# Kernel tuning notes

Hardware: AMD Instinct MI355X
Metric: run time of the kernel (lower is better)

The kernel has to match this reference:

```python
import jax, jax.numpy as jnp
import numpy as np
from jax import lax

N = 100000
G = 256          # voxel grid extent per axis
MULT = 8
C_HID = 32 * MULT  # 256
K3 = 27


def setup_inputs() -> dict:
    key = jax.random.key(0)
    k_feat, k1, k2, k3, k4 = jax.random.split(key, 5)
    # unique voxel coordinates in a G^3 grid (sparse tensors have no duplicate coords)
    rng = np.random.default_rng(0)
    lin = rng.choice(G * G * G, size=N, replace=False)
    coords = np.stack([lin // (G * G), (lin // G) % G, lin % G], axis=1).astype(np.int32)
    feats = jax.random.normal(k_feat, (N, 2), dtype=jnp.float32)
    def w(k, cin, cout):
        return jax.random.normal(k, (K3, cin, cout), dtype=jnp.float32) / np.sqrt(K3 * cin)
    return {
        "coords": jnp.asarray(coords),
        "feats": feats,
        "W1": w(k1, 2, C_HID),
        "W2": w(k2, C_HID, C_HID),
        "W3": w(k3, C_HID, C_HID),
        "W4": w(k4, C_HID, 2),
    }


def _neighbor_map(coords):
    """Kernel map for a 3x3x3 stride-1 sparse conv: for each of 27 offsets and each
    point i, the index j of the point at coords[i]+offset (and a validity mask).
    Built once and shared by all four layers (stride=1 preserves coordinates)."""
    S = G + 2  # pad linearization base so offsets in {-1,0,1} never wrap
    c = coords.astype(jnp.int32) + 1
    keys = (c[:, 0] * S + c[:, 1]) * S + c[:, 2]            # [N]
    order = jnp.argsort(keys)
    skeys = keys[order]
    offs = jnp.array([[dx, dy, dz] for dx in (-1, 0, 1)
                      for dy in (-1, 0, 1) for dz in (-1, 0, 1)], dtype=jnp.int32)  # [27,3]
    nc = c[None, :, :] + offs[:, None, :]                    # [27,N,3]
    qk = (nc[..., 0] * S + nc[..., 1]) * S + nc[..., 2]      # [27,N]
    pos = jnp.clip(jnp.searchsorted(skeys, qk), 0, N - 1)
    valid = skeys[pos] == qk                                 # [27,N]
    idx = order[pos]                                         # [27,N]
    return idx, valid


def _sparse_conv(feats, W, idx, valid):
    """gather -> GEMM -> accumulate, scanned over the 27 kernel offsets."""
    out0 = jnp.zeros((feats.shape[0], W.shape[-1]), feats.dtype)
    def step(acc, kv):
        i, v, w = kv
        g = jnp.where(v[:, None], feats[i], 0.0)   # [N,Cin] gathered neighbor feats
        return acc + g @ w, None
    out, _ = lax.scan(step, out0, (idx, valid, W))
    return out


def reference(coords, feats, W1, W2, W3, W4):
    idx, valid = _neighbor_map(coords)
    x = _sparse_conv(feats, W1, idx, valid)
    x = _sparse_conv(x, W2, idx, valid)
    x = _sparse_conv(x, W3, idx, valid)
    x = _sparse_conv(x, W4, idx, valid)
    return x
```

## Files before the change

### kernel.cpp

```cpp
#include <hip/hip_runtime.h>

#define HASH_BITS 19
#define HASH_SIZE (1u << HASH_BITS)
#define HASH_MASK (HASH_SIZE - 1)
#define EMPTY64 0xFFFFFFFFFFFFFFFFull
#define CH 256
#define PCH 32
#define NREP 8
#define NSEG (27 * NREP)
#define SEGCAP 4096
#define BM_WORDS 536704

typedef __attribute__((ext_vector_type(8))) short short8;
typedef __attribute__((ext_vector_type(4))) float floatx4;
typedef unsigned long long ull;

__device__ __forceinline__ unsigned cvt_pk_bf16(float a, float b) {
    unsigned r;
    asm("v_cvt_pk_bf16_f32 %0, %1, %2" : "=v"(r) : "v"(a), "v"(b));
    return r;
}

__device__ inline void split8_pack(const float* xa, uint4& hv, uint4& lv) {
#pragma unroll
    for (int p = 0; p < 4; ++p) {
        unsigned hp = cvt_pk_bf16(xa[2 * p], xa[2 * p + 1]);
        float h0 = __uint_as_float(hp << 16);
        float h1 = __uint_as_float(hp & 0xFFFF0000u);
        unsigned lp = cvt_pk_bf16(xa[2 * p] - h0, xa[2 * p + 1] - h1);
        ((unsigned*)&hv)[p] = hp;
        ((unsigned*)&lv)[p] = lp;
    }
}

__global__ void hash_insert_k(const int* __restrict__ coords, int n,
                              ull* __restrict__ tbl, unsigned* __restrict__ keys,
                              unsigned* __restrict__ bm) {
    int i = blockIdx.x * blockDim.x + threadIdx.x;
    if (i >= n) return;
    unsigned cx = (unsigned)(coords[3 * i + 0] + 1);
    unsigned cy = (unsigned)(coords[3 * i + 1] + 1);
    unsigned cz = (unsigned)(coords[3 * i + 2] + 1);
    unsigned key = (cx * 258u + cy) * 258u + cz;
    keys[i] = key;
    atomicOr(&bm[key >> 5], 1u << (key & 31));
    ull e = ((ull)key << 32) | (unsigned)i;
    unsigned h = (key * 2654435761u) & HASH_MASK;
    while (true) {
        ull prev = atomicCAS(&tbl[h], EMPTY64, e);
        if (prev == EMPTY64) return;
        h = (h + 1) & HASH_MASK;
    }
}

__global__ void neighbor_bm_k(const unsigned* __restrict__ keys, int n,
                              const unsigned* __restrict__ bm,
                              const ull* __restrict__ tbl,
                              int2* __restrict__ buckets, int* __restrict__ kcnt) {
    int t = blockIdx.x * blockDim.x + threadIdx.x;
    if (t >= n * 9) return;
    int rep = blockIdx.x & (NREP - 1);
    int i = t / 9, r = t - i * 9;
    unsigned key = keys[i];
    int base = (int)key + ((r / 3 - 1) * 258 + (r % 3 - 1)) * 258;
    unsigned bA = base - 1, bB = base, bC = base + 1;
    unsigned hit0 = (bm[bA >> 5] >> (bA & 31)) & 1u;
    unsigned hit1 = (bm[bB >> 5] >> (bB & 31)) & 1u;
    unsigned hit2 = (bm[bC >> 5] >> (bC & 31)) & 1u;
#pragma unroll
    for (int dz = -1; dz <= 1; ++dz) {
        if (r == 4 && dz == 0) continue;
        unsigned hit = dz < 0 ? hit0 : (dz == 0 ? hit1 : hit2);
        if (!hit) continue;
        unsigned nk = (unsigned)(base + dz);
        unsigned h = (nk * 2654435761u) & HASH_MASK;
        int j = -1;
        while (true) {
            ull e = tbl[h];
            if ((unsigned)(e >> 32) == nk) { j = (int)(e & 0xFFFFFFFFu); break; }
            if (e == EMPTY64) break;
            h = (h + 1) & HASH_MASK;
        }
        if (j >= 0) {
            int kk = 3 * r + dz + 1;
            int seg = kk * NREP + rep;
            int pos = atomicAdd(&kcnt[seg * 16], 1);
            buckets[(size_t)seg * SEGCAP + pos] = make_int2(i, j);
        }
    }
}

__global__ void chunk_desc_k(const int* __restrict__ kcnt,
                             int2* __restrict__ desc, int* __restrict__ nchunks) {
    __shared__ int cnts[NSEG];
    __shared__ int offs[NSEG + 1];
    int t = threadIdx.x;
    if (t < NSEG) cnts[t] = kcnt[t * 16];
    __syncthreads();
    if (t == 0) {
        int acc = 0;
        for (int s = 0; s < NSEG; ++s) { offs[s] = acc; acc += (cnts[s] + PCH - 1) / PCH; }
        offs[NSEG] = acc;
        *nchunks = acc;
    }
    __syncthreads();
    if (t < NSEG) {
        int cnt = cnts[t];
        int o = offs[t];
        int k = t / NREP;
        for (int c = 0; c * PCH < cnt; ++c) {
            int len = min(PCH, cnt - c * PCH);
            desc[o + c] = make_int2(t * SEGCAP + c * PCH, (k << 8) | len);
        }
    }
}

__global__ void prep_w_all_k(const float* __restrict__ W2, const float* __restrict__ W3,
                             unsigned short* __restrict__ Whi2, unsigned short* __restrict__ Wlo2,
                             unsigned short* __restrict__ Whi3, unsigned short* __restrict__ Wlo3) {
    int t = blockIdx.x * 256 + threadIdx.x;
    const int HALF = 27 * 8 * 256;
    if (t >= 2 * HALF) return;
    const float* W = (t < HALF) ? W2 : W3;
    unsigned short* Whi = (t < HALF) ? Whi2 : Whi3;
    unsigned short* Wlo = (t < HALF) ? Wlo2 : Wlo3;
    int tt = (t < HALF) ? t : t - HALF;
    int cout = tt & 255, kk = (tt >> 8) & 7, k = tt >> 11;
    int nt = cout >> 4, lc = cout & 15;
    const float* src = W + (size_t)k * 65536 + (size_t)kk * 32 * 256 + cout;
    size_t dbase = (((size_t)(k * 8 + kk) * 16 + nt) * 64 + lc) * 8;
#pragma unroll
    for (int kg = 0; kg < 4; ++kg) {
        float xa[8];
#pragma unroll
        for (int j = 0; j < 8; ++j) xa[j] = src[(size_t)(kg * 8 + j) * 256];
        uint4 hv, lv;
        split8_pack(xa, hv, lv);
        *(uint4*)(Whi + dbase + (size_t)kg * 16 * 8) = hv;
        *(uint4*)(Wlo + dbase + (size_t)kg * 16 * 8) = lv;
    }
}

__global__ void dense1_k(const float* __restrict__ x, const float* __restrict__ Wc,
                         float* __restrict__ out, int n) {
    int t = blockIdx.x * blockDim.x + threadIdx.x;
    if (t >= n * CH) return;
    int i = t >> 8, co = t & 255;
    float2 xv = *reinterpret_cast<const float2*>(x + 2 * i);
    out[t] = fmaf(xv.x, Wc[co], xv.y * Wc[CH + co]);
}

__global__ void sparse1b_k(const float* __restrict__ feats, const float* __restrict__ W1,
                           float* __restrict__ out, const int2* __restrict__ buckets,
                           const int2* __restrict__ desc, const int* __restrict__ nchunks) {
    __shared__ float xs[PCH][2];
    __shared__ int ii[PCH];
    int nc = *nchunks;
    int t = threadIdx.x;
    for (int m = blockIdx.x; m < nc; m += gridDim.x) {
        int2 d = desc[m];
        int k = d.y >> 8, len = d.y & 255;
        if (t < PCH) {
            if (t < len) {
                int2 pr = buckets[d.x + t];
                ii[t] = pr.x;
                xs[t][0] = feats[2 * pr.y];
                xs[t][1] = feats[2 * pr.y + 1];
            } else {
                ii[t] = -1;
                xs[t][0] = 0.f; xs[t][1] = 0.f;
            }
        }
        __syncthreads();
        const float* Wk = W1 + (size_t)k * 2 * CH;
        float w0 = Wk[t], w1 = Wk[CH + t];
#pragma unroll
        for (int p = 0; p < PCH; ++p) {
            int i = ii[p];
            if (i >= 0) atomicAdd(&out[(size_t)i * CH + t], fmaf(xs[p][0], w0, xs[p][1] * w1));
        }
        __syncthreads();
    }
}

__global__ __launch_bounds__(256, 3) void dense_mid_mfma_k(
        const float* __restrict__ x,
        const unsigned short* __restrict__ Whi,
        const unsigned short* __restrict__ Wlo,
        float* __restrict__ out, int n) {
    __shared__ unsigned short AsH[3][2048], AsL[3][2048];
    int t = threadIdx.x;
    int wid = t >> 6, lane = t & 63;
    int i0 = blockIdx.x * 64;

    floatx4 acc[4][4];
#pragma unroll
    for (int a = 0; a < 4; ++a)
#pragma unroll
        for (int b = 0; b < 4; ++b) acc[a][b] = floatx4{0.f, 0.f, 0.f, 0.f};

    int row = ((t >> 6) << 4) + (t & 15);
    int kg = (t >> 4) & 3;
    float sok = (i0 + row < n) ? 1.f : 0.f;
    const float* sp = x + (size_t)min(i0 + row, n - 1) * CH + kg * 8;

    floatx4 ra0, ra1;
    short8 Bh[2][4], Bl[2][4];

    auto loadB = [&](int kk, int b) {
#pragma unroll
        for (int q = 0; q < 4; ++q) {
            size_t off = (((size_t)kk * 16 + wid * 4 + q) * 64 + lane) * 8;
            Bh[b][q] = *(const short8*)&Whi[off];
            Bl[b][q] = *(const short8*)&Wlo[off];
        }
    };
    auto loadA = [&](int kk) {
        ra0 = *(const floatx4*)(sp + kk * 32);
        ra1 = *(const floatx4*)(sp + kk * 32 + 4);
    };
    auto writeA = [&](int bi) {
        float xa[8];
        xa[0] = ra0.x * sok; xa[1] = ra0.y * sok; xa[2] = ra0.z * sok; xa[3] = ra0.w * sok;
        xa[4] = ra1.x * sok; xa[5] = ra1.y * sok; xa[6] = ra1.z * sok; xa[7] = ra1.w * sok;
        uint4 hv, lv;
        split8_pack(xa, hv, lv);
        *(uint4*)&AsH[bi][t * 8] = hv;
        *(uint4*)&AsL[bi][t * 8] = lv;
    };
    auto compute = [&](int bi, int b) {
#pragma unroll
        for (int mt = 0; mt < 4; ++mt) {
            short8 ah = *(const short8*)&AsH[bi][(mt * 64 + lane) * 8];
            short8 al = *(const short8*)&AsL[bi][(mt * 64 + lane) * 8];
#pragma unroll
            for (int q = 0; q < 4; ++q) {
                acc[mt][q] = __builtin_amdgcn_mfma_f32_16x16x32_bf16(ah, Bh[b][q], acc[mt][q], 0, 0, 0);
                acc[mt][q] = __builtin_amdgcn_mfma_f32_16x16x32_bf16(al, Bh[b][q], acc[mt][q], 0, 0, 0);
                acc[mt][q] = __builtin_amdgcn_mfma_f32_16x16x32_bf16(ah, Bl[b][q], acc[mt][q], 0, 0, 0);
            }
        }
    };

    loadB(0, 0);
    loadA(0); writeA(0);
    loadA(1); writeA(1);
    __syncthreads();

#pragma unroll
    for (int kk = 0; kk < 8; ++kk) {
        if (kk < 7) loadB(kk + 1, (kk + 1) & 1);
        if (kk < 6) loadA(kk + 2);
        compute(kk % 3, kk & 1);
        if (kk < 6) writeA((kk + 2) % 3);
        __syncthreads();
    }

    int r0 = (lane >> 4) * 4, c0 = lane & 15;
#pragma unroll
    for (int mt = 0; mt < 4; ++mt)
#pragma unroll
        for (int r = 0; r < 4; ++r) {
            int orow = i0 + mt * 16 + r0 + r;
            if (orow < n) {
#pragma unroll
                for (int q = 0; q < 4; ++q)
                    out[(size_t)orow * CH + wid * 64 + q * 16 + c0] = acc[mt][q][r];
            }
        }
}

__global__ __launch_bounds__(256) void sparse_mid_mfma_k(
        const float* __restrict__ x,
        const unsigned short* __restrict__ Whi,
        const unsigned short* __restrict__ Wlo,
        float* __restrict__ out, const int2* __restrict__ buckets,
        const int2* __restrict__ desc, const int* __restrict__ nchunks) {
    __shared__ unsigned short As_hi[8192];
    __shared__ unsigned short As_lo[8192];
    __shared__ int ii[PCH];
    int nc = *nchunks;
    int t = threadIdx.x;
    int wid = t >> 6, lane = t & 63;
    int r = t >> 3, kk0 = t & 7;
    int mt_s = r >> 4, rl = r & 15;
    for (int m = blockIdx.x; m < nc; m += gridDim.x) {
        int2 d = desc[m];
        int k = d.y >> 8, len = d.y & 255;
        if (r < len) {
            int2 pr = buckets[d.x + r];
            if (kk0 == 0) ii[r] = pr.x;
            const float* src = x + (size_t)pr.y * CH + kk0 * 32;
#pragma unroll
            for (int kg = 0; kg < 4; ++kg) {
                float xa[8];
                floatx4 v0 = *(const floatx4*)(src + kg * 8);
                floatx4 v1 = *(const floatx4*)(src + kg * 8 + 4);
                xa[0] = v0.x; xa[1] = v0.y; xa[2] = v0.z; xa[3] = v0.w;
                xa[4] = v1.x; xa[5] = v1.y; xa[6] = v1.z; xa[7] = v1.w;
                uint4 hv, lv;
                split8_pack(xa, hv, lv);
                int ab = ((kk0 * 2 + mt_s) * 64 + kg * 16 + rl) * 8;
                *(uint4*)&As_hi[ab] = hv;
                *(uint4*)&As_lo[ab] = lv;
            }
        } else {
            if (kk0 == 0) ii[r] = -1;
            uint4 z = {0, 0, 0, 0};
#pragma unroll
            for (int kg = 0; kg < 4; ++kg) {
                int ab = ((kk0 * 2 + mt_s) * 64 + kg * 16 + rl) * 8;
                *(uint4*)&As_hi[ab] = z;
                *(uint4*)&As_lo[ab] = z;
            }
        }
        __syncthreads();
        floatx4 acc[2][4];
#pragma unroll
        for (int a = 0; a < 2; ++a)
#pragma unroll
            for (int b = 0; b < 4; ++b) acc[a][b] = floatx4{0.f, 0.f, 0.f, 0.f};

        short8 bh[2][4], bl[2][4];
        auto loadBs = [&](int kk, int b) {
#pragma unroll
            for (int q = 0; q < 4; ++q) {
                size_t off = (((size_t)(k * 8 + kk) * 16 + wid * 4 + q) * 64 + lane) * 8;
                bh[b][q] = *(const short8*)&Whi[off];
                bl[b][q] = *(const short8*)&Wlo[off];
            }
        };
        loadBs(0, 0);
#pragma unroll
        for (int kk = 0; kk < 8; ++kk) {
            if (kk < 7) loadBs(kk + 1, (kk + 1) & 1);
            int b = kk & 1;
            short8 ah0 = *(const short8*)&As_hi[((kk * 2 + 0) * 64 + lane) * 8];
            short8 al0 = *(const short8*)&As_lo[((kk * 2 + 0) * 64 + lane) * 8];
            short8 ah1 = *(const short8*)&As_hi[((kk * 2 + 1) * 64 + lane) * 8];
            short8 al1 = *(const short8*)&As_lo[((kk * 2 + 1) * 64 + lane) * 8];
#pragma unroll
            for (int q = 0; q < 4; ++q) {
                acc[0][q] = __builtin_amdgcn_mfma_f32_16x16x32_bf16(ah0, bh[b][q], acc[0][q], 0, 0, 0);
                acc[0][q] = __builtin_amdgcn_mfma_f32_16x16x32_bf16(al0, bh[b][q], acc[0][q], 0, 0, 0);
                acc[0][q] = __builtin_amdgcn_mfma_f32_16x16x32_bf16(ah0, bl[b][q], acc[0][q], 0, 0, 0);
                acc[1][q] = __builtin_amdgcn_mfma_f32_16x16x32_bf16(ah1, bh[b][q], acc[1][q], 0, 0, 0);
                acc[1][q] = __builtin_amdgcn_mfma_f32_16x16x32_bf16(al1, bh[b][q], acc[1][q], 0, 0, 0);
                acc[1][q] = __builtin_amdgcn_mfma_f32_16x16x32_bf16(ah1, bl[b][q], acc[1][q], 0, 0, 0);
            }
        }
        int r0 = (lane >> 4) * 4, c0 = lane & 15;
#pragma unroll
        for (int mt = 0; mt < 2; ++mt)
#pragma unroll
            for (int rr = 0; rr < 4; ++rr) {
                int orow = mt * 16 + r0 + rr;
                int i = ii[orow];
                if (i >= 0) {
#pragma unroll
                    for (int q = 0; q < 4; ++q)
                        atomicAdd(&out[(size_t)i * CH + wid * 64 + q * 16 + c0], acc[mt][q][rr]);
                }
            }
        __syncthreads();
    }
}

__device__ inline float wave_sum(float v) {
    for (int off = 32; off; off >>= 1) v += __shfl_xor(v, off);
    return v;
}

__global__ void dense4_k(const float* __restrict__ x, const float* __restrict__ Wc,
                         float* __restrict__ out, int n) {
    int wid = threadIdx.x >> 6, lane = threadIdx.x & 63;
    int i = blockIdx.x * 4 + wid;
    if (i >= n) return;
    floatx4 xv = *reinterpret_cast<const floatx4*>(x + (size_t)i * CH + lane * 4);
    floatx4 w0 = *reinterpret_cast<const floatx4*>(Wc + lane * 8);
    floatx4 w1 = *reinterpret_cast<const floatx4*>(Wc + lane * 8 + 4);
    float a0 = xv.x * w0.x + xv.y * w0.z + xv.z * w1.x + xv.w * w1.z;
    float a1 = xv.x * w0.y + xv.y * w0.w + xv.z * w1.y + xv.w * w1.w;
    a0 = wave_sum(a0);
    a1 = wave_sum(a1);
    if (lane == 0) { out[2 * i] = a0; out[2 * i + 1] = a1; }
}

__global__ void sparse4b_k(const float* __restrict__ x, const float* __restrict__ W4,
                           float* __restrict__ out, const int2* __restrict__ buckets,
                           const int2* __restrict__ desc, const int* __restrict__ nchunks) {
    int nc = *nchunks;
    int wid = threadIdx.x >> 6, lane = threadIdx.x & 63;
    for (int m = blockIdx.x; m < nc; m += gridDim.x) {
        int2 d = desc[m];
        int k = d.y >> 8, len = d.y & 255;
        const float* Wk = W4 + (size_t)k * CH * 2;
        floatx4 w0 = *reinterpret_cast<const floatx4*>(Wk + lane * 8);
        floatx4 w1 = *reinterpret_cast<const floatx4*>(Wk + lane * 8 + 4);
        for (int p = wid; p < len; p += 4) {
            int2 pr = buckets[d.x + p];
            floatx4 xv = *reinterpret_cast<const floatx4*>(x + (size_t)pr.y * CH + lane * 4);
            float a0 = xv.x * w0.x + xv.y * w0.z + xv.z * w1.x + xv.w * w1.z;
            float a1 = xv.x * w0.y + xv.y * w0.w + xv.z * w1.y + xv.w * w1.w;
            a0 = wave_sum(a0);
            a1 = wave_sum(a1);
            if (lane == 0) {
                atomicAdd(&out[2 * pr.x], a0);
                atomicAdd(&out[2 * pr.x + 1], a1);
            }
        }
    }
}

extern "C" void kernel_launch(void* const* d_in, const int* in_sizes, int n_in,
                              void* d_out, int out_size, void* d_ws, size_t ws_size,
                              hipStream_t stream) {
    const int* coords = (const int*)d_in[0];
    const float* feats = (const float*)d_in[1];
    const float* W1 = (const float*)d_in[2];
    const float* W2 = (const float*)d_in[3];
    const float* W3 = (const float*)d_in[4];
    const float* W4 = (const float*)d_in[5];
    float* out = (float*)d_out;
    int n = in_sizes[0] / 3;

    char* ws = (char*)d_ws;
    auto alloc = [&](size_t bytes) -> void* {
        void* p = (void*)ws;
        ws += (bytes + 255) & ~(size_t)255;
        return p;
    };
    ull* tbl = (ull*)alloc((size_t)HASH_SIZE * 8);
    unsigned* bm = (unsigned*)alloc((size_t)BM_WORDS * 4);
    int* kcnt = (int*)alloc((size_t)NSEG * 16 * 4);
    unsigned* keys = (unsigned*)alloc((size_t)n * 4);
    int* nchunks = (int*)alloc(4);
    int ndesc = NSEG * (SEGCAP / PCH);
    int2* desc = (int2*)alloc(sizeof(int2) * (size_t)ndesc);
    int2* buckets = (int2*)alloc(sizeof(int2) * (size_t)NSEG * SEGCAP);
    unsigned short* Whi2 = (unsigned short*)alloc((size_t)27 * 65536 * 2);
    unsigned short* Wlo2 = (unsigned short*)alloc((size_t)27 * 65536 * 2);
    unsigned short* Whi3 = (unsigned short*)alloc((size_t)27 * 65536 * 2);
    unsigned short* Wlo3 = (unsigned short*)alloc((size_t)27 * 65536 * 2);
    float* x1 = (float*)alloc((size_t)n * CH * 4);
    float* x2 = (float*)alloc((size_t)n * CH * 4);

    hipMemsetAsync(tbl, 0xFF, (size_t)HASH_SIZE * 8, stream);
    hipMemsetAsync(bm, 0, (size_t)BM_WORDS * 4 + (size_t)NSEG * 16 * 4, stream);

    hash_insert_k<<<(n + 255) / 256, 256, 0, stream>>>(coords, n, tbl, keys, bm);
    neighbor_bm_k<<<(n * 9 + 255) / 256, 256, 0, stream>>>(keys, n, bm, tbl, buckets, kcnt);
    chunk_desc_k<<<1, 256, 0, stream>>>(kcnt, desc, nchunks);
    prep_w_all_k<<<(2 * 27 * 8 * 256) / 256, 256, 0, stream>>>(W2, W3, Whi2, Wlo2, Whi3, Wlo3);

    int mtiles = (n + 63) / 64;

    dense1_k<<<(n * CH + 255) / 256, 256, 0, stream>>>(feats, W1 + 13 * 2 * CH, x1, n);
    sparse1b_k<<<1024, 256, 0, stream>>>(feats, W1, x1, buckets, desc, nchunks);

    dense_mid_mfma_k<<<mtiles, 256, 0, stream>>>(x1, Whi2 + (size_t)13 * 65536,
                                                 Wlo2 + (size_t)13 * 65536, x2, n);
    sparse_mid_mfma_k<<<512, 256, 0, stream>>>(x1, Whi2, Wlo2, x2, buckets, desc, nchunks);

    dense_mid_mfma_k<<<mtiles, 256, 0, stream>>>(x2, Whi3 + (size_t)13 * 65536,
                                                 Wlo3 + (size_t)13 * 65536, x1, n);
    sparse_mid_mfma_k<<<512, 256, 0, stream>>>(x2, Whi3, Wlo3, x1, buckets, desc, nchunks);

    dense4_k<<<(n + 3) / 4, 256, 0, stream>>>(x1, W4 + 13 * CH * 2, out, n);
    sparse4b_k<<<512, 256, 0, stream>>>(x1, W4, out, buckets, desc, nchunks);
}
```

Before: 282.2 us.

## Fuse front-end setup kernels and last-layer dense/sparse passes into single launches

```diff
diff --git a/kernel.cpp b/kernel.cpp
--- a/kernel.cpp
+++ b/kernel.cpp
@@ -3,13 +3,16 @@
 #define HASH_BITS 19
 #define HASH_SIZE (1u << HASH_BITS)
 #define HASH_MASK (HASH_SIZE - 1)
-#define EMPTY64 0xFFFFFFFFFFFFFFFFull
 #define CH 256
 #define PCH 32
 #define NREP 8
 #define NSEG (27 * NREP)
 #define SEGCAP 4096
 #define BM_WORDS 536704
+#define GD1 4096
+#define GH  391
+#define GD4 2048
+#define GS4 512
 
 typedef __attribute__((ext_vector_type(8))) short short8;
 typedef __attribute__((ext_vector_type(4))) float floatx4;
@@ -29,27 +32,82 @@
         float h1 = __uint_as_float(hp & 0xFFFF0000u);
         unsigned lp = cvt_pk_bf16(xa[2 * p] - h0, xa[2 * p + 1] - h1);
         ((unsigned*)&hv)[p] = hp;
-        ((unsigned*)&lv)[p] = lp;
-    }
-}
-
-__global__ void hash_insert_k(const int* __restrict__ coords, int n,
+        ((unsigned*)&lv)[p] = lv.x * 0 + lp;
+    }
+}
+
+__device__ inline void split8_pack2(const float* xa, uint4& hv, uint4& lv) {
+    unsigned hp[4], lp[4];
+#pragma unroll
+    for (int p = 0; p < 4; ++p) {
+        hp[p] = cvt_pk_bf16(xa[2 * p], xa[2 * p + 1]);
+        float h0 = __uint_as_float(hp[p] << 16);
+        float h1 = __uint_as_float(hp[p] & 0xFFFF0000u);
+        lp[p] = cvt_pk_bf16(xa[2 * p] - h0, xa[2 * p + 1] - h1);
+    }
+    hv.x = hp[0]; hv.y = hp[1]; hv.z = hp[2]; hv.w = hp[3];
+    lv.x = lp[0]; lv.y = lp[1]; lv.z = lp[2]; lv.w = lp[3];
+}
+
+__global__ void front_fused_k(const int* __restrict__ coords, int n, int gh,
                               ull* __restrict__ tbl, unsigned* __restrict__ keys,
-                              unsigned* __restrict__ bm) {
-    int i = blockIdx.x * blockDim.x + threadIdx.x;
-    if (i >= n) return;
-    unsigned cx = (unsigned)(coords[3 * i + 0] + 1);
-    unsigned cy = (unsigned)(coords[3 * i + 1] + 1);
-    unsigned cz = (unsigned)(coords[3 * i + 2] + 1);
-    unsigned key = (cx * 258u + cy) * 258u + cz;
-    keys[i] = key;
-    atomicOr(&bm[key >> 5], 1u << (key & 31));
-    ull e = ((ull)key << 32) | (unsigned)i;
-    unsigned h = (key * 2654435761u) & HASH_MASK;
-    while (true) {
-        ull prev = atomicCAS(&tbl[h], EMPTY64, e);
-        if (prev == EMPTY64) return;
-        h = (h + 1) & HASH_MASK;
+                              unsigned* __restrict__ bm,
+                              const float* __restrict__ feats, const float* __restrict__ W1c,
+                              float* __restrict__ x1,
+                              const float* __restrict__ W2, const float* __restrict__ W3,
+                              unsigned short* __restrict__ Whi2, unsigned short* __restrict__ Wlo2,
+                              unsigned short* __restrict__ Whi3, unsigned short* __restrict__ Wlo3) {
+    int b = blockIdx.x;
+    int t = threadIdx.x;
+    if (b < GD1) {
+        float w0 = W1c[t], w1 = W1c[CH + t];
+        for (int i = b; i < n; i += GD1) {
+            float2 xv = *reinterpret_cast<const float2*>(feats + 2 * i);
+            x1[(size_t)i * CH + t] = fmaf(xv.x, w0, xv.y * w1);
+        }
+        return;
+    }
+    b -= GD1;
+    if (b < gh) {
+        int i = b * 256 + t;
+        if (i >= n) return;
+        unsigned cx = (unsigned)(coords[3 * i + 0] + 1);
+        unsigned cy = (unsigned)(coords[3 * i + 1] + 1);
+        unsigned cz = (unsigned)(coords[3 * i + 2] + 1);
+        unsigned key = (cx * 258u + cy) * 258u + cz;
+        keys[i] = key;
+        atomicOr(&bm[key >> 5], 1u << (key & 31));
+        ull e = ((ull)key << 32) | (unsigned)i;
+        unsigned h = (key * 2654435761u) & HASH_MASK;
+        while (true) {
+            ull prev = atomicCAS(&tbl[h], 0ull, e);
+            if (prev == 0ull) return;
+            h = (h + 1) & HASH_MASK;
+        }
+    }
+    b -= gh;
+    {
+        int tt0 = b * 256 + t;
+        const int HALF = 27 * 8 * 256;
+        if (tt0 >= 2 * HALF) return;
+        const float* W = (tt0 < HALF) ? W2 : W3;
+        unsigned short* Whi = (tt0 < HALF) ? Whi2 : Whi3;
+        unsigned short* Wlo = (tt0 < HALF) ? Wlo2 : Wlo3;
+        int tt = (tt0 < HALF) ? tt0 : tt0 - HALF;
+        int cout = tt & 255, kk = (tt >> 8) & 7, k = tt >> 11;
+        int nt = cout >> 4, lc = cout & 15;
+        const float* src = W + (size_t)k * 65536 + (size_t)kk * 32 * 256 + cout;
+        size_t dbase = (((size_t)(k * 8 + kk) * 16 + nt) * 64 + lc) * 8;
+#pragma unroll
+        for (int kg = 0; kg < 4; ++kg) {
+            float xa[8];
+#pragma unroll
+            for (int j = 0; j < 8; ++j) xa[j] = src[(size_t)(kg * 8 + j) * 256];
+            uint4 hv, lv;
+            split8_pack2(xa, hv, lv);
+            *(uint4*)(Whi + dbase + (size_t)kg * 16 * 8) = hv;
+            *(uint4*)(Wlo + dbase + (size_t)kg * 16 * 8) = lv;
+        }
     }
 }
 
@@ -78,7 +136,7 @@
         while (true) {
             ull e = tbl[h];
             if ((unsigned)(e >> 32) == nk) { j = (int)(e & 0xFFFFFFFFu); break; }
-            if (e == EMPTY64) break;
+            if (e == 0ull) break;
             h = (h + 1) & HASH_MASK;
         }
         if (j >= 0) {
@@ -113,41 +171,6 @@
             desc[o + c] = make_int2(t * SEGCAP + c * PCH, (k << 8) | len);
         }
     }
-}
-
-__global__ void prep_w_all_k(const float* __restrict__ W2, const float* __restrict__ W3,
-                             unsigned short* __restrict__ Whi2, unsigned short* __restrict__ Wlo2,
-                             unsigned short* __restrict__ Whi3, unsigned short* __restrict__ Wlo3) {
-    int t = blockIdx.x * 256 + threadIdx.x;
-    const int HALF = 27 * 8 * 256;
-    if (t >= 2 * HALF) return;
-    const float* W = (t < HALF) ? W2 : W3;
-    unsigned short* Whi = (t < HALF) ? Whi2 : Whi3;
-    unsigned short* Wlo = (t < HALF) ? Wlo2 : Wlo3;
-    int tt = (t < HALF) ? t : t - HALF;
-    int cout = tt & 255, kk = (tt >> 8) & 7, k = tt >> 11;
-    int nt = cout >> 4, lc = cout & 15;
-    const float* src = W + (size_t)k * 65536 + (size_t)kk * 32 * 256 + cout;
-    size_t dbase = (((size_t)(k * 8 + kk) * 16 + nt) * 64 + lc) * 8;
-#pragma unroll
-    for (int kg = 0; kg < 4; ++kg) {
-        float xa[8];
-#pragma unroll
-        for (int j = 0; j < 8; ++j) xa[j] = src[(size_t)(kg * 8 + j) * 256];
-        uint4 hv, lv;
-        split8_pack(xa, hv, lv);
-        *(uint4*)(Whi + dbase + (size_t)kg * 16 * 8) = hv;
-        *(uint4*)(Wlo + dbase + (size_t)kg * 16 * 8) = lv;
-    }
-}
-
-__global__ void dense1_k(const float* __restrict__ x, const float* __restrict__ Wc,
-                         float* __restrict__ out, int n) {
-    int t = blockIdx.x * blockDim.x + threadIdx.x;
-    if (t >= n * CH) return;
-    int i = t >> 8, co = t & 255;
-    float2 xv = *reinterpret_cast<const float2*>(x + 2 * i);
-    out[t] = fmaf(xv.x, Wc[co], xv.y * Wc[CH + co]);
 }
 
 __global__ void sparse1b_k(const float* __restrict__ feats, const float* __restrict__ W1,
@@ -224,7 +247,7 @@
         xa[0] = ra0.x * sok; xa[1] = ra0.y * sok; xa[2] = ra0.z * sok; xa[3] = ra0.w * sok;
         xa[4] = ra1.x * sok; xa[5] = ra1.y * sok; xa[6] = ra1.z * sok; xa[7] = ra1.w * sok;
         uint4 hv, lv;
-        split8_pack(xa, hv, lv);
+        split8_pack2(xa, hv, lv);
         *(uint4*)&AsH[bi][t * 8] = hv;
         *(uint4*)&AsL[bi][t * 8] = lv;
     };
@@ -299,7 +322,7 @@
                 xa[0] = v0.x; xa[1] = v0.y; xa[2] = v0.z; xa[3] = v0.w;
                 xa[4] = v1.x; xa[5] = v1.y; xa[6] = v1.z; xa[7] = v1.w;
                 uint4 hv, lv;
-                split8_pack(xa, hv, lv);
+                split8_pack2(xa, hv, lv);
                 int ab = ((kk0 * 2 + mt_s) * 64 + kg * 16 + rl) * 8;
                 *(uint4*)&As_hi[ab] = hv;
                 *(uint4*)&As_lo[ab] = lv;
@@ -371,27 +394,32 @@
     return v;
 }
 
-__global__ void dense4_k(const float* __restrict__ x, const float* __restrict__ Wc,
-                         float* __restrict__ out, int n) {
+__global__ void back_fused_k(const float* __restrict__ x, const float* __restrict__ W4,
+                             float* __restrict__ out, int n,
+                             const int2* __restrict__ buckets,
+                             const int2* __restrict__ desc, const int* __restrict__ nchunks) {
+    int b = blockIdx.x;
     int wid = threadIdx.x >> 6, lane = threadIdx.x & 63;
-    int i = blockIdx.x * 4 + wid;
-    if (i >= n) return;
-    floatx4 xv = *reinterpret_cast<const floatx4*>(x + (size_t)i * CH + lane * 4);
-    floatx4 w0 = *reinterpret_cast<const floatx4*>(Wc + lane * 8);
-    floatx4 w1 = *reinterpret_cast<const floatx4*>(Wc + lane * 8 + 4);
-    float a0 = xv.x * w0.x + xv.y * w0.z + xv.z * w1.x + xv.w * w1.z;
-    float a1 = xv.x * w0.y + xv.y * w0.w + xv.z * w1.y + xv.w * w1.w;
-    a0 = wave_sum(a0);
-    a1 = wave_sum(a1);
-    if (lane == 0) { out[2 * i] = a0; out[2 * i + 1] = a1; }
-}
-
-__global__ void sparse4b_k(const float* __restrict__ x, const float* __restrict__ W4,
-                           float* __restrict__ out, const int2* __restrict__ buckets,
-                           const int2* __restrict__ desc, const int* __restrict__ nchunks) {
+    if (b < GD4) {
+        const float* Wc = W4 + 13 * CH * 2;
+        floatx4 w0 = *reinterpret_cast<const floatx4*>(Wc + lane * 8);
+        floatx4 w1 = *reinterpret_cast<const floatx4*>(Wc + lane * 8 + 4);
+        for (int i = b * 4 + wid; i < n; i += GD4 * 4) {
+            floatx4 xv = *reinterpret_cast<const floatx4*>(x + (size_t)i * CH + lane * 4);
+            float a0 = xv.x * w0.x + xv.y * w0.z + xv.z * w1.x + xv.w * w1.z;
+            float a1 = xv.x * w0.y + xv.y * w0.w + xv.z * w1.y + xv.w * w1.w;
+            a0 = wave_sum(a0);
+            a1 = wave_sum(a1);
+            if (lane == 0) {
+                atomicAdd(&out[2 * i], a0);
+                atomicAdd(&out[2 * i + 1], a1);
+            }
+        }
+        return;
+    }
+    b -= GD4;
     int nc = *nchunks;
-    int wid = threadIdx.x >> 6, lane = threadIdx.x & 63;
-    for (int m = blockIdx.x; m < nc; m += gridDim.x) {
+    for (int m = b; m < nc; m += GS4) {
         int2 d = desc[m];
         int k = d.y >> 8, len = d.y & 255;
         const float* Wk = W4 + (size_t)k * CH * 2;
@@ -445,18 +473,22 @@
     float* x1 = (float*)alloc((size_t)n * CH * 4);
     float* x2 = (float*)alloc((size_t)n * CH * 4);
 
-    hipMemsetAsync(tbl, 0xFF, (size_t)HASH_SIZE * 8, stream);
-    hipMemsetAsync(bm, 0, (size_t)BM_WORDS * 4 + (size_t)NSEG * 16 * 4, stream);
-
-    hash_insert_k<<<(n + 255) / 256, 256, 0, stream>>>(coords, n, tbl, keys, bm);
+    size_t zspan = (size_t)HASH_SIZE * 8 + (size_t)BM_WORDS * 4 + (size_t)NSEG * 16 * 4;
+    hipMemsetAsync(tbl, 0, zspan, stream);
+    hipMemsetAsync(out, 0, (size_t)out_size * 4, stream);
+
+    int gh = (n + 255) / 256;
+    int gp = (2 * 27 * 8 * 256) / 256;
+    front_fused_k<<<GD1 + gh + gp, 256, 0, stream>>>(
+        coords, n, gh, tbl, keys, bm,
+        feats, W1 + 13 * 2 * CH, x1,
+        W2, W3, Whi2, Wlo2, Whi3, Wlo3);
+
     neighbor_bm_k<<<(n * 9 + 255) / 256, 256, 0, stream>>>(keys, n, bm, tbl, buckets, kcnt);
     chunk_desc_k<<<1, 256, 0, stream>>>(kcnt, desc, nchunks);
-    prep_w_all_k<<<(2 * 27 * 8 * 256) / 256, 256, 0, stream>>>(W2, W3, Whi2, Wlo2, Whi3, Wlo3);
+    sparse1b_k<<<1024, 256, 0, stream>>>(feats, W1, x1, buckets, desc, nchunks);
 
     int mtiles = (n + 63) / 64;
-
-    dense1_k<<<(n * CH + 255) / 256, 256, 0, stream>>>(feats, W1 + 13 * 2 * CH, x1, n);
-    sparse1b_k<<<1024, 256, 0, stream>>>(feats, W1, x1, buckets, desc, nchunks);
 
     dense_mid_mfma_k<<<mtiles, 256, 0, stream>>>(x1, Whi2 + (size_t)13 * 65536,
                                                  Wlo2 + (size_t)13 * 65536, x2, n);
@@ -466,6 +498,5 @@
                                                  Wlo3 + (size_t)13 * 65536, x1, n);
     sparse_mid_mfma_k<<<512, 256, 0, stream>>>(x2, Whi3, Wlo3, x1, buckets, desc, nchunks);
 
-    dense4_k<<<(n + 3) / 4, 256, 0, stream>>>(x1, W4 + 13 * CH * 2, out, n);
-    sparse4b_k<<<512, 256, 0, stream>>>(x1, W4, out, buckets, desc, nchunks);
-}
+    back_fused_k<<<GD4 + GS4, 256, 0, stream>>>(x1, W4, out, n, buckets, desc, nchunks);
+}
```

Measured after the change: 252.6 us. 1.12x faster.
